# Kernel optimization log

Hardware: AMD Instinct MI355X
Metric: run time of the kernel (lower is better)

The kernel has to match this reference:

```python
import jax, jax.numpy as jnp
import numpy as np

HEAD_DIM = 128
Q_HEADS = 24
KV_HEADS = 8
TARGET_KV_HEADS = 32
HIDDEN = 3072


def setup_inputs() -> dict:
    key = jax.random.key(0)
    ks = jax.random.split(key, 8)
    bsz, q_len = 4, 2048
    return {
        "hidden_states": jax.random.normal(ks[0], (bsz, q_len, HIDDEN), jnp.float32),
        "rope_rotary_cos_sin": jax.random.normal(ks[1], (bsz, q_len, HEAD_DIM), jnp.float32),
        "context_lengths": jax.random.randint(ks[2], (bsz,), 0, q_len, jnp.int32),
        "kvcache_start_index": jax.random.randint(ks[3], (bsz,), 0, q_len, jnp.int32),
        "kv_cache": jax.random.normal(ks[4], (bsz, 2, KV_HEADS, 4096, HEAD_DIM), jnp.float32),
        "Wq": jax.random.normal(ks[5], (Q_HEADS * HEAD_DIM, HIDDEN), jnp.float32) * 0.02,
        "Wk": jax.random.normal(ks[6], (KV_HEADS * HEAD_DIM, HIDDEN), jnp.float32) * 0.02,
        "Wv": jax.random.normal(ks[7], (KV_HEADS * HEAD_DIM, HIDDEN), jnp.float32) * 0.02,
        "Wo": jax.random.normal(jax.random.fold_in(key, 99), (HIDDEN, Q_HEADS * HEAD_DIM), jnp.float32) * 0.02,
    }


def reference(hidden_states, rope_rotary_cos_sin, context_lengths, kvcache_start_index,
              kv_cache, Wq, Wk, Wv, Wo):
    bsz, q_len, _ = hidden_states.shape
    # QKV projections (nn.Linear, no bias): y = x @ W^T
    q = jnp.einsum('bsh,dh->bsd', hidden_states, Wq)
    k = jnp.einsum('bsh,dh->bsd', hidden_states, Wk)
    v = jnp.einsum('bsh,dh->bsd', hidden_states, Wv)
    # [b, heads, s, d]
    q = q.reshape(bsz, q_len, Q_HEADS, HEAD_DIM).transpose(0, 2, 1, 3)
    k = k.reshape(bsz, q_len, KV_HEADS, HEAD_DIM).transpose(0, 2, 1, 3)
    v = v.reshape(bsz, q_len, KV_HEADS, HEAD_DIM).transpose(0, 2, 1, 3)
    # GQA head padding: each kv head repeated `repeats` times contiguously
    repeats = TARGET_KV_HEADS // KV_HEADS
    k = jnp.repeat(k, repeats, axis=1)
    v = jnp.repeat(v, repeats, axis=1)
    qk_scale = jnp.asarray(HEAD_DIM ** -0.5, dtype=hidden_states.dtype)
    q = q * qk_scale
    # trt::fake_attention is a placeholder: returns (query.clone(), kv_cache.clone()).
    # Faithful to the source math: attn_output = scaled query; kv_cache passes through.
    attn_output = q  # [b, Q_HEADS, s, d]
    attn_output = attn_output.transpose(0, 2, 1, 3).reshape(bsz, q_len, Q_HEADS * HEAD_DIM)
    # current (3072) == o_proj.in_features (3072): no repeat/truncate branch taken
    out = jnp.einsum('bsd,od->bso', attn_output, Wo)
    return (out, kv_cache)
```

## Files before the change

### kernel.cpp

```cpp
#include <hip/hip_runtime.h>


typedef __attribute__((ext_vector_type(8))) __bf16 bf16x8;
typedef __attribute__((ext_vector_type(4))) float f32x4;

__device__ __forceinline__ unsigned short f2bf(float f) {
  union { float f; unsigned u; } v; v.f = f;
  unsigned r = v.u + 0x7fffu + ((v.u >> 16) & 1u);
  return (unsigned short)(r >> 16);
}

__device__ __forceinline__ ushort4 cast4(float4 v) {
  ushort4 o;
  o.x = f2bf(v.x); o.y = f2bf(v.y); o.z = f2bf(v.z); o.w = f2bf(v.w);
  return o;
}

typedef const __attribute__((address_space(1))) void* gptr_t;
typedef __attribute__((address_space(3))) void* lptr_t;

__device__ __forceinline__ void gload16(const void* g, void* l) {
  __builtin_amdgcn_global_load_lds((gptr_t)g, (lptr_t)l, 16, 0, 0);
}

#define BAR   do { asm volatile("" ::: "memory"); __builtin_amdgcn_s_barrier(); asm volatile("" ::: "memory"); } while (0)
#define LGKM0 asm volatile("s_waitcnt lgkmcnt(0)" ::: "memory")
#define VM(n) asm volatile("s_waitcnt vmcnt(" #n ")" ::: "memory")
#define PRIO1 __builtin_amdgcn_s_setprio(1)
#define PRIO0 __builtin_amdgcn_s_setprio(0)

__global__ __launch_bounds__(256)
void prep_fused(const float4* __restrict__ hs4, ushort4* __restrict__ Xb4,
                const float* __restrict__ Wq, ushort* __restrict__ WqT,
                const float4* __restrict__ Wo4, ushort4* __restrict__ Wob4,
                const float4* __restrict__ kv4, float4* __restrict__ kvd4) {
  __shared__ float tile[32][33];
  const int H = 3072;
  const int b = blockIdx.x;
  const int t = threadIdx.x;
  if (b < 4096) {
    if (kvd4) {
      const int base = b * 2048 + t;
#pragma unroll
      for (int k = 0; k < 8; ++k)
        kvd4[base + k * 256] = kv4[base + k * 256];
    }
  } else if (b < 6144) {
    const int base = (b - 4096) * 3072 + t;
#pragma unroll
    for (int k = 0; k < 12; ++k)
      Xb4[base + k * 256] = cast4(hs4[base + k * 256]);
  } else if (b < 15360) {
    const int id = b - 6144;
    const int tc = (id % 96) * 32;
    const int tr = (id / 96) * 32;
    const int lx = t & 31;
    const int ly = t >> 5;
#pragma unroll
    for (int i = 0; i < 32; i += 8)
      tile[ly + i][lx] = Wq[(size_t)(tr + ly + i) * H + (tc + lx)];
    __syncthreads();
#pragma unroll
    for (int i = 0; i < 32; i += 8)
      WqT[(size_t)(tc + ly + i) * H + (tr + lx)] = f2bf(tile[lx][ly + i]);
  } else {
    const int base = (b - 15360) * 2304 + t;
#pragma unroll
    for (int k = 0; k < 9; ++k)
      Wob4[base + k * 256] = cast4(Wo4[base + k * 256]);
  }
}

__global__ __launch_bounds__(512, 2)
void gemm8(const ushort* __restrict__ A, const ushort* __restrict__ B,
           float* __restrict__ C, int N, int K) {
  __shared__ __align__(16) char smem[131072];

  const int t    = threadIdx.x;
  const int w    = t >> 6;
  const int lane = t & 63;
  const int wr   = w >> 2;
  const int wc   = w & 3;
  const int fr   = lane & 15;
  const int g    = lane >> 4;

  const int nwg = gridDim.x;
  const int cpx = nwg >> 3;
  const int wg  = (blockIdx.x & 7) * cpx + (blockIdx.x >> 3);
  const int nbx = N >> 8;
  const int bx  = wg % nbx, by = wg / nbx;
  const int rowBase = by * 256, colBase = bx * 256;

  const int sr   = t >> 3;
  const int scol = ((t & 7) ^ (sr & 7)) << 3;
  const ushort* Ag = A + (size_t)(rowBase + sr) * K + scol;
  const ushort* Bg = B + (size_t)(colBase + sr) * K + scol;
  const int wofs = w << 10;

#define BUF(T) (((T) & 1) * 65536)
#define STG(half_base, srcp, kt) do {                                   \
    char* d_ = smem + (half_base) + wofs;                               \
    const ushort* s_ = (srcp) + (size_t)(kt) * 64;                      \
    gload16(s_, d_); gload16(s_ + (size_t)64 * K, d_ + 8192); } while (0)
#define SA_LO(kt) STG(BUF(kt) +     0, Ag,                  kt)
#define SA_HI(kt) STG(BUF(kt) + 16384, Ag + (size_t)128 * K, kt)
#define SB_LO(kt) STG(BUF(kt) + 32768, Bg,                  kt)
#define SB_HI(kt) STG(BUF(kt) + 49152, Bg + (size_t)128 * K, kt)

  const int cs0 = (g ^ (fr & 7)) << 4;
  const int cs1 = ((4 | g) ^ (fr & 7)) << 4;
  const int aB  = wr * 16384 + fr * 128;
  const int bB  = 32768 + (wc >> 1) * 16384 + (wc & 1) * 8192 + fr * 128;

#define RD_A(bo, MH) do {                                               \
    const char* p_ = smem + (bo) + aB + (MH) * 8192;                    \
    a8[0] = *(const bf16x8*)(p_ + cs0);                                 \
    a8[1] = *(const bf16x8*)(p_ + 2048 + cs0);                          \
    a8[2] = *(const bf16x8*)(p_ + 4096 + cs0);                          \
    a8[3] = *(const bf16x8*)(p_ + 6144 + cs0);                          \
    a8[4] = *(const bf16x8*)(p_ + cs1);                                 \
    a8[5] = *(const bf16x8*)(p_ + 2048 + cs1);                          \
    a8[6] = *(const bf16x8*)(p_ + 4096 + cs1);                          \
    a8[7] = *(const bf16x8*)(p_ + 6144 + cs1); } while (0)
#define RD_B(dst, bo, NH) do {                                          \
    const char* p_ = smem + (bo) + bB + (NH) * 4096;                    \
    dst[0] = *(const bf16x8*)(p_ + cs0);                                \
    dst[1] = *(const bf16x8*)(p_ + 2048 + cs0);                         \
    dst[2] = *(const bf16x8*)(p_ + cs1);                                \
    dst[3] = *(const bf16x8*)(p_ + 2048 + cs1); } while (0)
#define MF16(MH, NH, bq) do {                                           \
    _Pragma("unroll") for (int mi_ = 0; mi_ < 4; ++mi_)                 \
    _Pragma("unroll") for (int ni_ = 0; ni_ < 2; ++ni_) {               \
      acc[(MH)*4+mi_][(NH)*2+ni_] = __builtin_amdgcn_mfma_f32_16x16x32_bf16( \
          a8[mi_], bq[ni_], acc[(MH)*4+mi_][(NH)*2+ni_], 0, 0, 0);      \
      acc[(MH)*4+mi_][(NH)*2+ni_] = __builtin_amdgcn_mfma_f32_16x16x32_bf16( \
          a8[4+mi_], bq[2+ni_], acc[(MH)*4+mi_][(NH)*2+ni_], 0, 0, 0); } } while (0)

  f32x4 acc[8][4];
#pragma unroll
  for (int m = 0; m < 8; ++m)
#pragma unroll
    for (int n = 0; n < 4; ++n)
      acc[m][n] = f32x4{0.f, 0.f, 0.f, 0.f};

  bf16x8 a8[8], Bq0[4], Bq1[4];

  const int nt = K >> 6;

  SA_LO(0); SA_HI(0); SB_LO(0); SB_HI(0);
  SB_LO(1); SB_HI(1);
  VM(4);
  BAR;

  for (int it = 0; it < nt / 2; ++it) {
    const int T   = 2 * it;
    const int bo0 = BUF(T), bo1 = BUF(T + 1);
    const bool s2 = (T + 2) < nt;
    RD_A(bo0, 0); RD_B(Bq0, bo0, 0);
    SA_LO(T + 1);
    BAR; LGKM0; PRIO1; MF16(0, 0, Bq0); PRIO0; BAR;
    RD_B(Bq1, bo0, 1);
    SA_HI(T + 1);
    BAR; LGKM0; PRIO1; MF16(0, 1, Bq1); PRIO0; BAR;
    RD_A(bo0, 1);
    if (s2) SB_LO(T + 2);
    BAR; LGKM0; PRIO1; MF16(1, 1, Bq1); PRIO0; BAR;
    if (s2) SB_HI(T + 2);
    BAR; LGKM0; PRIO1; MF16(1, 0, Bq0); PRIO0;
    if (s2) { VM(4); } else { VM(0); }
    BAR;
    RD_A(bo1, 0); RD_B(Bq0, bo1, 0);
    if (s2) SA_LO(T + 2);
    BAR; LGKM0; PRIO1; MF16(0, 0, Bq0); PRIO0; BAR;
    RD_B(Bq1, bo1, 1);
    if (s2) SA_HI(T + 2);
    BAR; LGKM0; PRIO1; MF16(0, 1, Bq1); PRIO0; BAR;
    RD_A(bo1, 1);
    if (s2) SB_LO(T + 3);
    BAR; LGKM0; PRIO1; MF16(1, 1, Bq1); PRIO0; BAR;
    if (s2) SB_HI(T + 3);
    BAR; LGKM0; PRIO1; MF16(1, 0, Bq0); PRIO0;
    if (s2) VM(4);
    BAR;
  }

#undef BUF
#undef STG
#undef SA_LO
#undef SA_HI
#undef SB_LO
#undef SB_HI
#undef RD_A
#undef RD_B
#undef MF16

  const int ocol = colBase + wc * 64 + fr;
#pragma unroll
  for (int r = 0; r < 8; ++r) {
    const int orow = rowBase + wr * 128 + (r >> 2) * 64 + (r & 3) * 16 + (g << 2);
#pragma unroll
    for (int c = 0; c < 4; ++c) {
      const int col = ocol + (c >> 1) * 32 + (c & 1) * 16;
#pragma unroll
      for (int i = 0; i < 4; ++i)
        C[(size_t)(orow + i) * N + col] = acc[r][c][i];
    }
  }
}

template <int OUT_BF16>
__global__ __launch_bounds__(256, 2)
void gemm_n(const ushort* __restrict__ A, const ushort* __restrict__ B,
            void* __restrict__ Cv, int N, int K, float scale) {
  __shared__ __align__(16) char smem[81920];

  const int t    = threadIdx.x;
  const int w    = t >> 6;
  const int lane = t & 63;
  const int wr   = w >> 1;
  const int wc   = w & 1;
  const int fr   = lane & 15;
  const int g    = lane >> 4;

  const int nwg = gridDim.x;
  const int cpx = nwg >> 3;
  const int wg  = (blockIdx.x & 7) * cpx + (blockIdx.x >> 3);
  const int nbx = N / 192;
  const int bx  = wg % nbx, by = wg / nbx;
  const int rowBase = by * 128, colBase = bx * 192;

  const int sr   = lane >> 3;
  const int scol = ((lane & 7) ^ sr) << 3;
  const ushort* Ag = A + (size_t)(rowBase + w * 8 + sr) * K + scol;
  const ushort* Bg = B + (size_t)(colBase + w * 8 + sr) * K + scol;
  const int wofs = w << 10;

#define SLOT(T) (((T) & 1) * 40960)
#define STAGE(kt) do {                                                  \
    char* d_ = smem + SLOT(kt) + wofs;                                  \
    const ushort* sa_ = Ag + (size_t)(kt) * 64;                         \
    gload16(sa_,                    d_);                                \
    gload16(sa_ + (size_t)32 * K,   d_ + 4096);                         \
    gload16(sa_ + (size_t)64 * K,   d_ + 8192);                         \
    gload16(sa_ + (size_t)96 * K,   d_ + 12288);                        \
    const ushort* sb_ = Bg + (size_t)(kt) * 64;                         \
    gload16(sb_,                    d_ + 16384);                        \
    gload16(sb_ + (size_t)32 * K,   d_ + 20480);                        \
    gload16(sb_ + (size_t)64 * K,   d_ + 24576);                        \
    gload16(sb_ + (size_t)96 * K,   d_ + 28672);                        \
    gload16(sb_ + (size_t)128 * K,  d_ + 32768);                        \
    gload16(sb_ + (size_t)160 * K,  d_ + 36864); } while (0)

  const int aBase = (wr * 64 + fr) * 128;
  const int bBase = 16384 + (wc * 96 + fr) * 128;
  const int cs0   = (g ^ (fr & 7)) << 4;
  const int cs1   = ((4 | g) ^ (fr & 7)) << 4;

#define READ_A(dst, so, CS) do {                                        \
    const char* p_ = smem + (so) + aBase + (CS);                        \
    dst[0] = *(const bf16x8*)(p_);                                      \
    dst[1] = *(const bf16x8*)(p_ + 2048);                               \
    dst[2] = *(const bf16x8*)(p_ + 4096);                               \
    dst[3] = *(const bf16x8*)(p_ + 6144); } while (0)
#define READ_B(dst, so, CS) do {                                        \
    const char* p_ = smem + (so) + bBase + (CS);                        \
    dst[0] = *(const bf16x8*)(p_);                                      \
    dst[1] = *(const bf16x8*)(p_ + 2048);                               \
    dst[2] = *(const bf16x8*)(p_ + 4096);                               \
    dst[3] = *(const bf16x8*)(p_ + 6144);                               \
    dst[4] = *(const bf16x8*)(p_ + 8192);                               \
    dst[5] = *(const bf16x8*)(p_ + 10240); } while (0)
#define MFMA24(A4, B6) do {                                             \
    _Pragma("unroll") for (int mi_ = 0; mi_ < 4; ++mi_)                 \
    _Pragma("unroll") for (int ni_ = 0; ni_ < 6; ++ni_)                 \
      acc[mi_][ni_] = __builtin_amdgcn_mfma_f32_16x16x32_bf16(          \
          A4[mi_], B6[ni_], acc[mi_][ni_], 0, 0, 0); } while (0)

  f32x4 acc[4][6];
#pragma unroll
  for (int m = 0; m < 4; ++m)
#pragma unroll
    for (int n = 0; n < 6; ++n)
      acc[m][n] = f32x4{0.f, 0.f, 0.f, 0.f};

  bf16x8 Af[4], Bf[6];

  const int nt = K >> 6;

  STAGE(0);
  VM(0);
  BAR;

  for (int T = 0; T < nt; ++T) {
    const int so = SLOT(T);
    READ_A(Af, so, cs0);
    READ_B(Bf, so, cs0);
    if (T + 1 < nt) STAGE(T + 1);
    LGKM0;
    PRIO1; MFMA24(Af, Bf); PRIO0;
    READ_A(Af, so, cs1);
    READ_B(Bf, so, cs1);
    LGKM0;
    PRIO1; MFMA24(Af, Bf); PRIO0;
    VM(0);
    BAR;
  }

#undef STAGE
#undef READ_A
#undef READ_B
#undef MFMA24
#undef SLOT

  const int orow = rowBase + wr * 64 + (g << 2);
  const int ocol = colBase + wc * 96 + fr;
#pragma unroll
  for (int mi = 0; mi < 4; ++mi)
#pragma unroll
    for (int ni = 0; ni < 6; ++ni)
#pragma unroll
      for (int i = 0; i < 4; ++i) {
        const size_t idx = (size_t)(orow + mi * 16 + i) * N + (ocol + ni * 16);
        float v = acc[mi][ni][i] * scale;
        if (OUT_BF16) ((ushort*)Cv)[idx] = f2bf(v);
        else          ((float*)Cv)[idx]  = v;
      }
}

extern "C" void kernel_launch(void* const* d_in, const int* in_sizes, int n_in,
                              void* d_out, int out_size, void* d_ws, size_t ws_size,
                              hipStream_t stream) {
  const float* hs = (const float*)d_in[0];
  const float* kv = (const float*)d_in[4];
  const float* Wq = (const float*)d_in[5];
  const float* Wo = (const float*)d_in[8];

  const int M = 8192, H = 3072;
  const int OUT_ELEMS = M * H;
  const int nkv = in_sizes[4];

  float* out = (float*)d_out;

  ushort* Xb   = (ushort*)d_ws;
  ushort* Wob  = Xb + (size_t)M * H;
  ushort* WqTb = Wob + (size_t)H * H;
  const size_t WS_NEED = 2ull * ((size_t)M * H + 3ull * (size_t)H * H);
  const bool ws_ok = ws_size >= WS_NEED;
  ushort* Wb = ws_ok ? (WqTb + (size_t)H * H) : (ushort*)(out + OUT_ELEMS);

  const float qk_scale = 0.08838834764831845f;

  const float4* kvs = ws_ok ? (const float4*)kv : nullptr;
  float4* kvd = ws_ok ? (float4*)(out + OUT_ELEMS) : nullptr;
  prep_fused<<<16384, 256, 0, stream>>>((const float4*)hs, (ushort4*)Xb,
                                        Wq, WqTb, (const float4*)Wo,
                                        (ushort4*)Wob, kvs, kvd);

  gemm_n<1><<<(H / 128) * (H / 192), 256, 0, stream>>>(
      Wob, WqTb, (void*)Wb, H, H, qk_scale);

  gemm8<<<(M / 256) * (H / 256), 512, 0, stream>>>(Xb, Wb, out, H, H);

  if (!ws_ok) {
    hipMemcpyAsync(out + OUT_ELEMS, kv, (size_t)nkv * sizeof(float),
                   hipMemcpyDeviceToDevice, stream);
  }
}
```

Baseline: 321.2 us.

## Triple-buffer A tiles in main GEMM to prefetch two k-steps ahead

```diff
diff --git a/kernel.cpp b/kernel.cpp
--- a/kernel.cpp
+++ b/kernel.cpp
@@ -72,9 +72,9 @@
 }
 
 __global__ __launch_bounds__(512, 2)
-void gemm8(const ushort* __restrict__ A, const ushort* __restrict__ B,
-           float* __restrict__ C, int N, int K) {
-  __shared__ __align__(16) char smem[131072];
+void gemm8b(const ushort* __restrict__ A, const ushort* __restrict__ B,
+            float* __restrict__ C, int N, int K) {
+  __shared__ __align__(16) char smem[163840];
 
   const int t    = threadIdx.x;
   const int w    = t >> 6;
@@ -97,23 +97,18 @@
   const ushort* Bg = B + (size_t)(colBase + sr) * K + scol;
   const int wofs = w << 10;
 
-#define BUF(T) (((T) & 1) * 65536)
-#define STG(half_base, srcp, kt) do {                                   \
-    char* d_ = smem + (half_base) + wofs;                               \
+#define STG(base, srcp, kt) do {                                        \
+    char* d_ = smem + (base) + wofs;                                    \
     const ushort* s_ = (srcp) + (size_t)(kt) * 64;                      \
     gload16(s_, d_); gload16(s_ + (size_t)64 * K, d_ + 8192); } while (0)
-#define SA_LO(kt) STG(BUF(kt) +     0, Ag,                  kt)
-#define SA_HI(kt) STG(BUF(kt) + 16384, Ag + (size_t)128 * K, kt)
-#define SB_LO(kt) STG(BUF(kt) + 32768, Bg,                  kt)
-#define SB_HI(kt) STG(BUF(kt) + 49152, Bg + (size_t)128 * K, kt)
 
   const int cs0 = (g ^ (fr & 7)) << 4;
   const int cs1 = ((4 | g) ^ (fr & 7)) << 4;
-  const int aB  = wr * 16384 + fr * 128;
-  const int bB  = 32768 + (wc >> 1) * 16384 + (wc & 1) * 8192 + fr * 128;
+  const int aBl = wr * 16384 + fr * 128;
+  const int bBl = (wc >> 1) * 16384 + (wc & 1) * 8192 + fr * 128;
 
 #define RD_A(bo, MH) do {                                               \
-    const char* p_ = smem + (bo) + aB + (MH) * 8192;                    \
+    const char* p_ = smem + (bo) + aBl + (MH) * 8192;                   \
     a8[0] = *(const bf16x8*)(p_ + cs0);                                 \
     a8[1] = *(const bf16x8*)(p_ + 2048 + cs0);                          \
     a8[2] = *(const bf16x8*)(p_ + 4096 + cs0);                          \
@@ -123,7 +118,7 @@
     a8[6] = *(const bf16x8*)(p_ + 4096 + cs1);                          \
     a8[7] = *(const bf16x8*)(p_ + 6144 + cs1); } while (0)
 #define RD_B(dst, bo, NH) do {                                          \
-    const char* p_ = smem + (bo) + bB + (NH) * 4096;                    \
+    const char* p_ = smem + (bo) + bBl + (NH) * 4096;                   \
     dst[0] = *(const bf16x8*)(p_ + cs0);                                \
     dst[1] = *(const bf16x8*)(p_ + 2048 + cs0);                         \
     dst[2] = *(const bf16x8*)(p_ + cs1);                                \
@@ -147,49 +142,37 @@
 
   const int nt = K >> 6;
 
-  SA_LO(0); SA_HI(0); SB_LO(0); SB_HI(0);
-  SB_LO(1); SB_HI(1);
-  VM(4);
+  STG(0,      Ag,                   0); STG(16384,          Ag + (size_t)128 * K, 0);
+  STG(98304,  Bg,                   0); STG(98304 + 16384,  Bg + (size_t)128 * K, 0);
+  STG(32768,  Ag,                   1); STG(32768 + 16384,  Ag + (size_t)128 * K, 1);
+  STG(131072, Bg,                   1); STG(131072 + 16384, Bg + (size_t)128 * K, 1);
+  VM(8);
   BAR;
 
-  for (int it = 0; it < nt / 2; ++it) {
-    const int T   = 2 * it;
-    const int bo0 = BUF(T), bo1 = BUF(T + 1);
+  int a_rd = 0, a_st = 2;
+  for (int T = 0; T < nt; ++T) {
+    const int boA = a_rd * 32768;
+    const int boB = 98304 + (T & 1) * 32768;
+    const int stA = a_st * 32768;
     const bool s2 = (T + 2) < nt;
-    RD_A(bo0, 0); RD_B(Bq0, bo0, 0);
-    SA_LO(T + 1);
+    RD_A(boA, 0); RD_B(Bq0, boB, 0);
+    if (s2) STG(stA, Ag, T + 2);
     BAR; LGKM0; PRIO1; MF16(0, 0, Bq0); PRIO0; BAR;
-    RD_B(Bq1, bo0, 1);
-    SA_HI(T + 1);
+    RD_B(Bq1, boB, 1);
+    if (s2) STG(stA + 16384, Ag + (size_t)128 * K, T + 2);
     BAR; LGKM0; PRIO1; MF16(0, 1, Bq1); PRIO0; BAR;
-    RD_A(bo0, 1);
-    if (s2) SB_LO(T + 2);
+    RD_A(boA, 1);
+    if (s2) STG(boB, Bg, T + 2);
     BAR; LGKM0; PRIO1; MF16(1, 1, Bq1); PRIO0; BAR;
-    if (s2) SB_HI(T + 2);
+    if (s2) STG(boB + 16384, Bg + (size_t)128 * K, T + 2);
     BAR; LGKM0; PRIO1; MF16(1, 0, Bq0); PRIO0;
-    if (s2) { VM(4); } else { VM(0); }
+    if (s2) { VM(8); } else { VM(0); }
     BAR;
-    RD_A(bo1, 0); RD_B(Bq0, bo1, 0);
-    if (s2) SA_LO(T + 2);
-    BAR; LGKM0; PRIO1; MF16(0, 0, Bq0); PRIO0; BAR;
-    RD_B(Bq1, bo1, 1);
-    if (s2) SA_HI(T + 2);
-    BAR; LGKM0; PRIO1; MF16(0, 1, Bq1); PRIO0; BAR;
-    RD_A(bo1, 1);
-    if (s2) SB_LO(T + 3);
-    BAR; LGKM0; PRIO1; MF16(1, 1, Bq1); PRIO0; BAR;
-    if (s2) SB_HI(T + 3);
-    BAR; LGKM0; PRIO1; MF16(1, 0, Bq0); PRIO0;
-    if (s2) VM(4);
-    BAR;
-  }
-
-#undef BUF
+    a_rd = (a_rd == 2) ? 0 : a_rd + 1;
+    a_st = (a_st == 2) ? 0 : a_st + 1;
+  }
+
 #undef STG
-#undef SA_LO
-#undef SA_HI
-#undef SB_LO
-#undef SB_HI
 #undef RD_A
 #undef RD_B
 #undef MF16
@@ -359,7 +342,7 @@
   gemm_n<1><<<(H / 128) * (H / 192), 256, 0, stream>>>(
       Wob, WqTb, (void*)Wb, H, H, qk_scale);
 
-  gemm8<<<(M / 256) * (H / 256), 512, 0, stream>>>(Xb, Wb, out, H, H);
+  gemm8b<<<(M / 256) * (H / 256), 512, 0, stream>>>(Xb, Wb, out, H, H);
 
   if (!ws_ok) {
     hipMemcpyAsync(out + OUT_ELEMS, kv, (size_t)nkv * sizeof(float),
```

Measured after the change: 332.7 us. +3.6%, slower.
